# Performance work log

Hardware: AMD Instinct MI355X
Metric: run time of the kernel (lower is better)

The kernel has to match this reference:

```python
import jax, jax.numpy as jnp
import numpy as np

N = 40000          # nodes
E = 640000         # edges (avg degree 16)
D_MODEL = 128
H = 8              # num_heads
DH = 16            # d_head
DFF = 512
CLAMP = 5.0
EPS = 1e-5


def setup_inputs() -> dict:
    key = jax.random.key(0)
    ks = jax.random.split(key, 10)
    s = 0.08  # weight init scale
    return {
        "feat": jax.random.normal(ks[0], (N, D_MODEL), dtype=jnp.float32),
        "src": jax.random.randint(ks[1], (E,), 0, N, dtype=jnp.int32),
        "dst": jax.random.randint(ks[2], (E,), 0, N, dtype=jnp.int32),
        "Wq": jax.random.normal(ks[3], (H * DH, D_MODEL), dtype=jnp.float32) * s,
        "Wk": jax.random.normal(ks[4], (H * DH, D_MODEL), dtype=jnp.float32) * s,
        "Wv": jax.random.normal(ks[5], (H * DH, D_MODEL), dtype=jnp.float32) * s,
        "Wo": jax.random.normal(ks[6], (D_MODEL, H * DH), dtype=jnp.float32) * s,
        "ln1_g": jnp.ones((D_MODEL,), jnp.float32),
        "ln1_b": jnp.zeros((D_MODEL,), jnp.float32),
        "W1": jax.random.normal(ks[7], (DFF, D_MODEL), dtype=jnp.float32) * s,
        "b1": jnp.zeros((DFF,), jnp.float32),
        "W2": jax.random.normal(ks[8], (D_MODEL, DFF), dtype=jnp.float32) * s,
        "b2": jnp.zeros((D_MODEL,), jnp.float32),
        "ln2_g": jnp.ones((D_MODEL,), jnp.float32),
        "ln2_b": jnp.zeros((D_MODEL,), jnp.float32),
    }


def _layer_norm(x, g, b):
    mu = jnp.mean(x, axis=-1, keepdims=True)
    var = jnp.mean(jnp.square(x - mu), axis=-1, keepdims=True)
    return (x - mu) * jax.lax.rsqrt(var + EPS) * g + b


def reference(feat, src, dst, Wq, Wk, Wv, Wo, ln1_g, ln1_b, W1, b1, W2, b2, ln2_g, ln2_b):
    n = feat.shape[0]
    # Node-level projections (equivalent to DGL's per-edge Linear on gathered feats)
    q = (feat @ Wq.T).reshape(n, H, DH)
    k = (feat @ Wk.T).reshape(n, H, DH)
    v = (feat @ Wv.T).reshape(n, H, DH)

    # Per-edge multi-head attention logits: q[dst] . k[src] / sqrt(d_head), clamped
    u = jnp.sum(q[dst] * k[src], axis=-1) / np.sqrt(DH)   # [E, H]
    u = jnp.clip(u, -CLAMP, CLAMP)

    # Ragged edge-softmax over incoming edges of each dst node
    m = jax.ops.segment_max(u, dst, num_segments=n)        # [N, H]
    e = jnp.exp(u - m[dst])                                # [E, H]
    denom = jax.ops.segment_sum(e, dst, num_segments=n)    # [N, H]
    a = e / denom[dst]                                     # [E, H]

    # Weighted V scatter-reduce back to dst nodes
    av = (a[:, :, None] * v[src]).reshape(-1, H * DH)      # [E, H*DH]
    sum_av = jax.ops.segment_sum(av, dst, num_segments=n)  # [N, H*DH]
    uh = sum_av @ Wo.T                                     # [N, d_model]

    h1 = _layer_norm(feat + uh, ln1_g, ln1_b)
    ffn = jax.nn.relu(h1 @ W1.T + b1) @ W2.T + b2
    return _layer_norm(h1 + ffn, ln2_g, ln2_b)
```

## Files before the change

kernel.cpp:

```cpp
#include <hip/hip_runtime.h>

#define DM 128
#define DFF 512
#define CLAMP_V 5.0f
#define LN_EPS 1e-5f

typedef __attribute__((ext_vector_type(8))) short bf16x8;
typedef __attribute__((ext_vector_type(4))) float f32x4;

__device__ __forceinline__ float b2f(ushort u) {
  union { uint u; float f; } x; x.u = ((uint)u) << 16; return x.f;
}
__device__ __forceinline__ ushort f2b(float f) {
  union { float f; uint u; } x; x.f = f;
  uint r = x.u + 0x7FFFu + ((x.u >> 16) & 1u);
  return (ushort)(r >> 16);
}
__device__ __forceinline__ void unpackw(uint w, float& lo, float& hi) {
  union { uint u; float f; } A, B;
  A.u = w << 16; B.u = w & 0xFFFF0000u;
  lo = A.f; hi = B.f;
}
__device__ __forceinline__ void unpack8w(uint4 w, float* o) {
  unpackw(w.x, o[0], o[1]); unpackw(w.y, o[2], o[3]);
  unpackw(w.z, o[4], o[5]); unpackw(w.w, o[6], o[7]);
}

__global__ void k_prep(const float* __restrict__ feat,
                       const float* __restrict__ wq, const float* __restrict__ wk,
                       const float* __restrict__ wv, const float* __restrict__ wo,
                       const float* __restrict__ w1, const float* __restrict__ w2,
                       ushort* __restrict__ feat_bf, ushort* __restrict__ wbf,
                       const int* __restrict__ dst, int* __restrict__ deg,
                       int nf4, int castBlocks, int E) {
  if ((int)blockIdx.x >= castBlocks) {
    int e = ((int)blockIdx.x - castBlocks) * 256 + threadIdx.x;
    if (e < E) atomicAdd(&deg[dst[e]], 1);
    return;
  }
  int i = blockIdx.x * 256 + threadIdx.x;
  if (i < nf4) {
    float4 v = *reinterpret_cast<const float4*>(feat + i * 4);
    ushort4 o; o.x = f2b(v.x); o.y = f2b(v.y); o.z = f2b(v.z); o.w = f2b(v.w);
    *reinterpret_cast<ushort4*>(feat_bf + i * 4) = o;
    return;
  }
  int i4 = (i - nf4) * 4;
  if (i4 >= 196608) return;
  const float* s; int o;
  if      (i4 < 16384)  { s = wq; o = i4; }
  else if (i4 < 32768)  { s = wk; o = i4 - 16384; }
  else if (i4 < 49152)  { s = wv; o = i4 - 32768; }
  else if (i4 < 65536)  { s = wo; o = i4 - 49152; }
  else if (i4 < 131072) { s = w1; o = i4 - 65536; }
  else                  { s = w2; o = i4 - 131072; }
  float4 v = *reinterpret_cast<const float4*>(s + o);
  ushort4 u; u.x = f2b(v.x); u.y = f2b(v.y); u.z = f2b(v.z); u.w = f2b(v.w);
  *reinterpret_cast<ushort4*>(wbf + i4) = u;
}

#define SC_EPB 1024

__global__ __launch_bounds__(256) void k_scan(const int* __restrict__ deg,
                                              int* __restrict__ off,
                                              int* __restrict__ cur,
                                              int n, int E) {
  __shared__ int sh[256];
  __shared__ int wsum[4];
  const int t = threadIdx.x;
  const int bstart = blockIdx.x * SC_EPB;

  int gs = 0;
  for (int base = t * 4; base < bstart; base += SC_EPB) {
    int4 v = *reinterpret_cast<const int4*>(deg + base);
    gs += v.x + v.y + v.z + v.w;
  }
  #pragma unroll
  for (int m = 1; m < 64; m <<= 1) gs += __shfl_xor(gs, m);
  if ((t & 63) == 0) wsum[t >> 6] = gs;
  __syncthreads();
  int gadd = wsum[0] + wsum[1] + wsum[2] + wsum[3];
  __syncthreads();

  int base = bstart + t * 4;
  int4 v = {0, 0, 0, 0};
  if (base + 3 < n) {
    v = *reinterpret_cast<const int4*>(deg + base);
  } else {
    if (base     < n) v.x = deg[base];
    if (base + 1 < n) v.y = deg[base + 1];
    if (base + 2 < n) v.z = deg[base + 2];
    if (base + 3 < n) v.w = deg[base + 3];
  }
  int s = v.x + v.y + v.z + v.w;
  sh[t] = s;
  __syncthreads();
  #pragma unroll
  for (int d = 1; d < 256; d <<= 1) {
    int x = 0;
    if (t >= d) x = sh[t - d];
    __syncthreads();
    sh[t] += x;
    __syncthreads();
  }
  int ex = sh[t] - s + gadd;
  if (base + 3 < n) {
    int4 o; o.x = ex; o.y = ex + v.x; o.z = ex + v.x + v.y; o.w = ex + v.x + v.y + v.z;
    *reinterpret_cast<int4*>(off + base) = o;
    int4 z = {0, 0, 0, 0};
    *reinterpret_cast<int4*>(cur + base) = z;
  } else {
    if (base     < n) { off[base]     = ex;                    cur[base]     = 0; }
    if (base + 1 < n) { off[base + 1] = ex + v.x;              cur[base + 1] = 0; }
    if (base + 2 < n) { off[base + 2] = ex + v.x + v.y;        cur[base + 2] = 0; }
    if (base + 3 < n) { off[base + 3] = ex + v.x + v.y + v.z;  cur[base + 3] = 0; }
  }
  if (blockIdx.x == 0 && t == 0) off[n] = E;
}

__global__ void k_scatter(const int* __restrict__ src, const int* __restrict__ dst,
                          const int* __restrict__ off, int* __restrict__ cur,
                          int* __restrict__ csr, int E) {
  int e = blockIdx.x * blockDim.x + threadIdx.x;
  if (e < E) {
    int d = dst[e];
    int p = off[d] + atomicAdd(&cur[d], 1);
    csr[p] = src[e];
  }
}

template<int FLAGS>
__global__ __launch_bounds__(512, 2) void k_mmT(
    const ushort* __restrict__ A, const ushort* __restrict__ W,
    ushort* __restrict__ Cb, ushort* __restrict__ Cb2, int M)
{
  __shared__ ushort As[128 * 128];
  __shared__ ushort Bs[128 * 128];

  const int tid = threadIdx.x;
  const int wv = tid >> 6, ln = tid & 63;
  const int bnb = blockIdx.x;
  const int mbase = blockIdx.y * 128;
  const int wrow = (wv >> 2) * 64, wcol = (wv & 3) * 32;
  const int o_base = tid * 16;

  #pragma unroll
  for (int is = 0; is < 4; ++is) {
    int o = is * 8192 + o_base;
    int row = o >> 8;
    int c = ((o >> 4) & 15) ^ (row & 15);
    int gr = min(mbase + row, M - 1);
    const ushort* sA = A + (size_t)gr * 128 + c * 8;
    __builtin_amdgcn_global_load_lds(
        (const __attribute__((address_space(1))) void*)sA,
        (__attribute__((address_space(3))) void*)((char*)As + is * 8192 + wv * 1024),
        16, 0, 0);
    const ushort* sB = W + (size_t)(bnb * 128 + row) * 128 + c * 8;
    __builtin_amdgcn_global_load_lds(
        (const __attribute__((address_space(1))) void*)sB,
        (__attribute__((address_space(3))) void*)((char*)Bs + is * 8192 + wv * 1024),
        16, 0, 0);
  }
  __syncthreads();

  f32x4 acc[4][2] = {};
  const char* AsB = (const char*)As;
  const char* BsB = (const char*)Bs;
  #pragma unroll
  for (int kk = 0; kk < 4; ++kk) {
    bf16x8 af[4], bfr[2];
    #pragma unroll
    for (int m = 0; m < 4; ++m) {
      int r = wrow + m * 16 + (ln & 15);
      int c = kk * 4 + (ln >> 4);
      af[m] = *reinterpret_cast<const bf16x8*>(AsB + r * 256 + ((c ^ (r & 15)) << 4));
    }
    #pragma unroll
    for (int n = 0; n < 2; ++n) {
      int r = wcol + n * 16 + (ln & 15);
      int c = kk * 4 + (ln >> 4);
      bfr[n] = *reinterpret_cast<const bf16x8*>(BsB + r * 256 + ((c ^ (r & 15)) << 4));
    }
    #pragma unroll
    for (int m = 0; m < 4; ++m)
      #pragma unroll
      for (int n = 0; n < 2; ++n)
        acc[m][n] = __builtin_amdgcn_mfma_f32_16x16x32_bf16(af[m], bfr[n], acc[m][n], 0, 0, 0);
  }

  #pragma unroll
  for (int m = 0; m < 4; ++m) {
    int gr0 = mbase + wrow + m * 16 + (ln >> 4) * 4;
    #pragma unroll
    for (int n = 0; n < 2; ++n) {
      int gcl = wcol + n * 16 + (ln & 15);
      #pragma unroll
      for (int r = 0; r < 4; ++r) {
        int gr = gr0 + r;
        if (gr >= M) continue;
        float v = acc[m][n][r];
        if (bnb == 0) Cb[(size_t)gr * 128 + gcl] = f2b(v);
        else          Cb2[(size_t)gr * 256 + (bnb - 1) * 128 + gcl] = f2b(v);
      }
    }
  }
}

__global__ __launch_bounds__(512, 2) void k_fused(
    const ushort* __restrict__ sav, const float* __restrict__ feat,
    const ushort* __restrict__ wo,
    const float* __restrict__ ln1g, const float* __restrict__ ln1b,
    const ushort* __restrict__ w1, const float* __restrict__ b1,
    const ushort* __restrict__ w2, const float* __restrict__ b2,
    const float* __restrict__ ln2g, const float* __restrict__ ln2b,
    float* __restrict__ outp, int M)
{
  __shared__ ushort mid[64 * 512];
  __shared__ ushort wbuf[2][128 * 128];

  const int tid = threadIdx.x;
  const int wv = tid >> 6, ln = tid & 63;
  const int lr = ln & 15, hi = ln >> 4;
  const int mbase = blockIdx.x * 64;
  char* M0 = (char*)mid;
  char* M1 = (char*)mid + 16384;
  char* M2 = (char*)mid + 32768;

  auto STG128 = [&](const ushort* srcBase, int srcLd, int colOff, char* dstLds) {
    #pragma unroll
    for (int is = 0; is < 4; ++is) {
      int o = is * 8192 + tid * 16;
      int r = o >> 8;
      int c = ((o >> 4) & 15) ^ (r & 15);
      const ushort* s = srcBase + (size_t)r * srcLd + colOff + c * 8;
      __builtin_amdgcn_global_load_lds(
          (const __attribute__((address_space(1))) void*)s,
          (__attribute__((address_space(3))) void*)(dstLds + is * 8192 + wv * 1024),
          16, 0, 0);
    }
  };

  #pragma unroll
  for (int is = 0; is < 2; ++is) {
    int o = is * 8192 + tid * 16;
    int r = o >> 8;
    int c = ((o >> 4) & 15) ^ (r & 15);
    int gr = min(mbase + r, M - 1);
    const ushort* s = sav + (size_t)gr * 128 + c * 8;
    __builtin_amdgcn_global_load_lds(
        (const __attribute__((address_space(1))) void*)s,
        (__attribute__((address_space(3))) void*)(M1 + is * 8192 + wv * 1024),
        16, 0, 0);
  }
  STG128(wo, 128, 0, (char*)wbuf[0]);
  STG128(w1, 128, 0, M2);
  __syncthreads();

  const int gc = wv * 16 + lr;

  f32x4 p0[4] = {};
  {
    const char* wB = (const char*)wbuf[0];
    #pragma unroll
    for (int kk = 0; kk < 4; ++kk) {
      int c = kk * 4 + hi;
      int wr = wv * 16 + lr;
      bf16x8 bWo = *reinterpret_cast<const bf16x8*>(wB + wr * 256 + ((c ^ (wr & 15)) << 4));
      bf16x8 aS[4];
      #pragma unroll
      for (int m = 0; m < 4; ++m) {
        int r = m * 16 + lr;
        aS[m] = *reinterpret_cast<const bf16x8*>(M1 + r * 256 + ((c ^ (r & 15)) << 4));
      }
      #pragma unroll
      for (int m = 0; m < 4; ++m)
        p0[m] = __builtin_amdgcn_mfma_f32_16x16x32_bf16(aS[m], bWo, p0[m], 0, 0, 0);
    }
  }
  #pragma unroll
  for (int m = 0; m < 4; ++m)
    #pragma unroll
    for (int r = 0; r < 4; ++r) {
      int gr = mbase + m * 16 + hi * 4 + r;
      p0[m][r] += feat[(size_t)min(gr, M - 1) * 128 + gc];
    }
  float* lnred = reinterpret_cast<float*>(&wbuf[1][0]);
  #pragma unroll
  for (int m = 0; m < 4; ++m)
    #pragma unroll
    for (int r = 0; r < 4; ++r) {
      float sm = p0[m][r];
      float sq = p0[m][r] * p0[m][r];
      #pragma unroll
      for (int msk = 1; msk <= 8; msk <<= 1) {
        sm += __shfl_xor(sm, msk);
        sq += __shfl_xor(sq, msk);
      }
      if (lr == 0) {
        int row = m * 16 + hi * 4 + r;
        lnred[row * 16 + wv * 2]     = sm;
        lnred[row * 16 + wv * 2 + 1] = sq;
      }
    }
  __syncthreads();
  STG128(w1 + 16384, 128, 0, (char*)wbuf[0]);
  {
    float g1v = ln1g[gc], bb1 = ln1b[gc];
    int chunk = gc >> 3;
    int sub = (gc & 7) * 2;
    #pragma unroll
    for (int m = 0; m < 4; ++m)
      #pragma unroll
      for (int r = 0; r < 4; ++r) {
        int row = m * 16 + hi * 4 + r;
        float sm = 0.f, sq = 0.f;
        #pragma unroll
        for (int w = 0; w < 8; ++w) {
          sm += lnred[row * 16 + w * 2];
          sq += lnred[row * 16 + w * 2 + 1];
        }
        float mu = sm * (1.f / 128.f);
        float var = fmaxf(sq * (1.f / 128.f) - mu * mu, 0.f);
        float rstd = rsqrtf(var + LN_EPS);
        float y = (p0[m][r] - mu) * rstd * g1v + bb1;
        p0[m][r] = y;
        *reinterpret_cast<ushort*>(M0 + row * 256 + ((chunk ^ (row & 15)) << 4) + sub) = f2b(y);
      }
  }
  __syncthreads();

  f32x4 p1[4][4] = {};
  #pragma unroll
  for (int g = 0; g < 4; ++g) {
    if (g == 0) STG128(w1 + 2 * 16384, 128, 0, (char*)wbuf[1]);
    if (g == 1) STG128(w1 + 3 * 16384, 128, 0, M2);
    if (g == 2) STG128(w2, 512, 0,   (char*)wbuf[0]);
    if (g == 3) STG128(w2, 512, 128, (char*)wbuf[1]);
    const char* wB = (g == 0) ? M2
                   : (g == 1) ? (const char*)wbuf[0]
                   : (g == 2) ? (const char*)wbuf[1]
                   : M2;
    #pragma unroll
    for (int kk = 0; kk < 4; ++kk) {
      int c = kk * 4 + hi;
      int wr = wv * 16 + lr;
      bf16x8 aW = *reinterpret_cast<const bf16x8*>(wB + wr * 256 + ((c ^ (wr & 15)) << 4));
      bf16x8 bH[4];
      #pragma unroll
      for (int hj = 0; hj < 4; ++hj) {
        int r = hj * 16 + lr;
        bH[hj] = *reinterpret_cast<const bf16x8*>(M0 + r * 256 + ((c ^ (r & 15)) << 4));
      }
      #pragma unroll
      for (int hj = 0; hj < 4; ++hj)
        p1[g][hj] = __builtin_amdgcn_mfma_f32_16x16x32_bf16(aW, bH[hj], p1[g][hj], 0, 0, 0);
    }
    __syncthreads();
  }

  #pragma unroll
  for (int g = 0; g < 4; ++g) {
    int mc0 = g * 128 + wv * 16 + hi * 4;
    float4 bv = *reinterpret_cast<const float4*>(b1 + mc0);
    int chunk = mc0 >> 3;
    int sub = (mc0 & 7) * 2;
    #pragma unroll
    for (int hj = 0; hj < 4; ++hj) {
      int orow = hj * 16 + lr;
      ushort4 pk;
      pk.x = f2b(fmaxf(p1[g][hj][0] + bv.x, 0.f));
      pk.y = f2b(fmaxf(p1[g][hj][1] + bv.y, 0.f));
      pk.z = f2b(fmaxf(p1[g][hj][2] + bv.z, 0.f));
      pk.w = f2b(fmaxf(p1[g][hj][3] + bv.w, 0.f));
      char* dstp = (char*)mid + orow * 1024 + (((chunk & 63) ^ (orow & 15)) << 4) + sub;
      *reinterpret_cast<ushort4*>(dstp) = pk;
    }
  }
  __syncthreads();

  f32x4 p2[4] = {};
  #pragma unroll
  for (int g2 = 0; g2 < 4; ++g2) {
    if (g2 == 1) STG128(w2, 512, 256, (char*)wbuf[0]);
    if (g2 == 2) STG128(w2, 512, 384, (char*)wbuf[1]);
    const char* wB = (const char*)wbuf[g2 & 1];
    #pragma unroll
    for (int kk = 0; kk < 4; ++kk) {
      int wr = wv * 16 + lr;
      int cw = kk * 4 + hi;
      bf16x8 bW = *reinterpret_cast<const bf16x8*>(wB + wr * 256 + ((cw ^ (wr & 15)) << 4));
      int cm = g2 * 16 + kk * 4 + hi;
      bf16x8 aM[4];
      #pragma unroll
      for (int m = 0; m < 4; ++m) {
        int r = m * 16 + lr;
        aM[m] = *reinterpret_cast<const bf16x8*>((const char*)mid + r * 1024 + (((cm & 63) ^ (r & 15)) << 4));
      }
      #pragma unroll
      for (int m = 0; m < 4; ++m)
        p2[m] = __builtin_amdgcn_mfma_f32_16x16x32_bf16(aM[m], bW, p2[m], 0, 0, 0);
    }
    __syncthreads();
  }

  lnred = reinterpret_cast<float*>(&wbuf[0][0]);
  {
    float bsv = b2[gc];
    #pragma unroll
    for (int m = 0; m < 4; ++m)
      #pragma unroll
      for (int r = 0; r < 4; ++r)
        p2[m][r] += bsv + p0[m][r];
  }
  #pragma unroll
  for (int m = 0; m < 4; ++m)
    #pragma unroll
    for (int r = 0; r < 4; ++r) {
      float sm = p2[m][r];
      float sq = p2[m][r] * p2[m][r];
      #pragma unroll
      for (int msk = 1; msk <= 8; msk <<= 1) {
        sm += __shfl_xor(sm, msk);
        sq += __shfl_xor(sq, msk);
      }
      if (lr == 0) {
        int row = m * 16 + hi * 4 + r;
        lnred[row * 16 + wv * 2]     = sm;
        lnred[row * 16 + wv * 2 + 1] = sq;
      }
    }
  __syncthreads();
  {
    float g2v = ln2g[gc], bb2 = ln2b[gc];
    #pragma unroll
    for (int m = 0; m < 4; ++m)
      #pragma unroll
      for (int r = 0; r < 4; ++r) {
        int row = m * 16 + hi * 4 + r;
        int gr = mbase + row;
        float sm = 0.f, sq = 0.f;
        #pragma unroll
        for (int w = 0; w < 8; ++w) {
          sm += lnred[row * 16 + w * 2];
          sq += lnred[row * 16 + w * 2 + 1];
        }
        float mu = sm * (1.f / 128.f);
        float var = fmaxf(sq * (1.f / 128.f) - mu * mu, 0.f);
        float rstd = rsqrtf(var + LN_EPS);
        if (gr < M)
          outp[(size_t)gr * 128 + gc] = (p2[m][r] - mu) * rstd * g2v + bb2;
      }
  }
}

__global__ __launch_bounds__(256) void k_attn(
    const ushort* __restrict__ q, const ushort* __restrict__ kv,
    const int* __restrict__ off, const int* __restrict__ csr,
    ushort* __restrict__ sav, int n)
{
  int node = blockIdx.x * 4 + (threadIdx.x >> 6);
  int lane = threadIdx.x & 63;
  if (node >= n) return;
  const int g = lane >> 3, sl = lane & 7;

  const ushort* qr = q + (size_t)node * 128 + sl * 16;
  uint4 qw0 = *reinterpret_cast<const uint4*>(qr);
  uint4 qw1 = *reinterpret_cast<const uint4*>(qr + 8);
  float qv[16];
  unpack8w(qw0, qv); unpack8w(qw1, qv + 8);

  int b = off[node], e = off[node + 1];
  float s = 0.f;
  float a[16] = {};
  int nIt = (e - b + 7) >> 3;
  int idx = b + g;
  int sn = (b < e) ? csr[min(idx, e - 1)] : 0;

  for (int i = 0; i < nIt; ++i) {
    bool act = idx < e;
    const ushort* kr = kv + (size_t)sn * 256 + sl * 16;
    uint4 kw0 = *reinterpret_cast<const uint4*>(kr);
    uint4 kw1 = *reinterpret_cast<const uint4*>(kr + 8);
    uint4 vw0 = *reinterpret_cast<const uint4*>(kr + 128);
    uint4 vw1 = *reinterpret_cast<const uint4*>(kr + 136);
    idx += 8;
    if (i + 1 < nIt) sn = csr[min(idx, e - 1)];

    float kk[16];
    unpack8w(kw0, kk); unpack8w(kw1, kk + 8);
    float p = 0.f;
    #pragma unroll
    for (int j = 0; j < 16; ++j) p = fmaf(qv[j], kk[j], p);
    float u = fminf(fmaxf(p * 0.25f, -CLAMP_V), CLAMP_V);
    float w = __expf(u - CLAMP_V);
    w = act ? w : 0.f;
    s += w;
    float vvv[16];
    unpack8w(vw0, vvv); unpack8w(vw1, vvv + 8);
    #pragma unroll
    for (int j = 0; j < 16; ++j) a[j] = fmaf(w, vvv[j], a[j]);
  }

  #pragma unroll
  for (int msk = 8; msk <= 32; msk <<= 1) {
    s += __shfl_xor(s, msk);
    #pragma unroll
    for (int j = 0; j < 16; ++j) a[j] += __shfl_xor(a[j], msk);
  }

  float inv = (s > 0.f) ? 1.f / s : 0.f;
  if (g == 0) {
    uint w[8];
    #pragma unroll
    for (int j = 0; j < 8; ++j)
      w[j] = (uint)f2b(a[2 * j] * inv) | ((uint)f2b(a[2 * j + 1] * inv) << 16);
    ushort* outp = sav + (size_t)node * 128 + sl * 16;
    uint4 o0 = {w[0], w[1], w[2], w[3]};
    uint4 o1 = {w[4], w[5], w[6], w[7]};
    *reinterpret_cast<uint4*>(outp) = o0;
    *reinterpret_cast<uint4*>(outp + 8) = o1;
  }
}

extern "C" void kernel_launch(void* const* d_in, const int* in_sizes, int n_in,
                              void* d_out, int out_size, void* d_ws, size_t ws_size,
                              hipStream_t stream)
{
  const float* feat = (const float*)d_in[0];
  const int*   src  = (const int*)d_in[1];
  const int*   dst  = (const int*)d_in[2];
  const float* Wq   = (const float*)d_in[3];
  const float* Wk   = (const float*)d_in[4];
  const float* Wv   = (const float*)d_in[5];
  const float* Wo   = (const float*)d_in[6];
  const float* ln1g = (const float*)d_in[7];
  const float* ln1b = (const float*)d_in[8];
  const float* W1   = (const float*)d_in[9];
  const float* b1   = (const float*)d_in[10];
  const float* W2   = (const float*)d_in[11];
  const float* b2   = (const float*)d_in[12];
  const float* ln2g = (const float*)d_in[13];
  const float* ln2b = (const float*)d_in[14];
  float* out = (float*)d_out;

  const int N = in_sizes[0] / DM;
  const int E = in_sizes[1];
  const size_t NB = (size_t)N;

  char* wsb = (char*)d_ws;
  ushort* q_bf    = (ushort*)wsb;
  ushort* kv_bf   = (ushort*)(wsb + NB * 256);
  ushort* sav_bf  = (ushort*)(wsb + NB * 768);
  ushort* feat_bf = (ushort*)(wsb + NB * 1792);
  ushort* wbf     = (ushort*)(wsb + NB * 2048);
  ushort* wqkv_bf = wbf;
  ushort* wo_bf   = wbf + 49152;
  ushort* w1_bf   = wbf + 65536;
  ushort* w2_bf   = wbf + 131072;
  int* ib  = (int*)(wbf + 196608);
  int* deg = ib;
  int* cur = ib + N;
  int* off = ib + 2 * N;
  int* csr = ib + 3 * N + 1;

  hipMemsetAsync(deg, 0, (size_t)N * sizeof(int), stream);

  int nf4 = N * DM / 4;
  int castBlocks = (nf4 + 49152 + 255) / 256;
  int cntBlocks = (E + 255) / 256;
  k_prep<<<castBlocks + cntBlocks, 256, 0, stream>>>(
      feat, Wq, Wk, Wv, Wo, W1, W2, feat_bf, wbf, dst, deg, nf4, castBlocks, E);

  int nbk = (N + SC_EPB - 1) / SC_EPB;
  k_scan<<<nbk, 256, 0, stream>>>(deg, off, cur, N, E);
  k_scatter<<<cntBlocks, 256, 0, stream>>>(src, dst, off, cur, csr, E);

  int nb4 = (N + 3) / 4;
  const int nT = (N + 127) / 128;

  k_mmT<0><<<dim3(3, nT), 512, 0, stream>>>(feat_bf, wqkv_bf, q_bf, kv_bf, N);

  k_attn<<<nb4, 256, 0, stream>>>(q_bf, kv_bf, off, csr, sav_bf, N);

  const int nF = (N + 63) / 64;
  k_fused<<<nF, 512, 0, stream>>>(
      sav_bf, feat, wo_bf, ln1g, ln1b, w1_bf, b1, w2_bf, b2, ln2g, ln2b, out, N);
}
```

Baseline: 196.8 us.

## Merge CSR scatter into QKV GEMM, split out-proj+LN1 kernel, packed-f32 attention

The CSR scatter pass now runs as extra blocks of the QKV projection launch, which removes one kernel launch and lets the two overlap. The Wo projection, residual add and LayerNorm1 move out of the fused FFN kernel into a separate GEMM+LN kernel with 128-row tiles, which writes h1 in bf16. The FFN kernel then reads h1 back and uses a simpler double-buffered weight staging. The attention inner loop is rewritten with float2 vectors so the compiler can emit packed FP32 FMAs. The split adds a global round-trip of h1 and an extra launch, and using the bf16 h1 as the residual slightly changes numerics.

```diff
diff --git a/kernel.cpp b/kernel.cpp
--- a/kernel.cpp
+++ b/kernel.cpp
@@ -7,6 +7,7 @@
 
 typedef __attribute__((ext_vector_type(8))) short bf16x8;
 typedef __attribute__((ext_vector_type(4))) float f32x4;
+typedef __attribute__((ext_vector_type(2))) float f32x2;
 
 __device__ __forceinline__ float b2f(ushort u) {
   union { uint u; float f; } x; x.u = ((uint)u) << 16; return x.f;
@@ -16,14 +17,10 @@
   uint r = x.u + 0x7FFFu + ((x.u >> 16) & 1u);
   return (ushort)(r >> 16);
 }
-__device__ __forceinline__ void unpackw(uint w, float& lo, float& hi) {
-  union { uint u; float f; } A, B;
-  A.u = w << 16; B.u = w & 0xFFFF0000u;
-  lo = A.f; hi = B.f;
-}
-__device__ __forceinline__ void unpack8w(uint4 w, float* o) {
-  unpackw(w.x, o[0], o[1]); unpackw(w.y, o[2], o[3]);
-  unpackw(w.z, o[4], o[5]); unpackw(w.w, o[6], o[7]);
+__device__ __forceinline__ f32x2 upk2(uint w) {
+  union { uint u; float f; } a, b;
+  a.u = w << 16; b.u = w & 0xFFFF0000u;
+  f32x2 r; r[0] = a.f; r[1] = b.f; return r;
 }
 
 __global__ void k_prep(const float* __restrict__ feat,
@@ -118,29 +115,30 @@
   if (blockIdx.x == 0 && t == 0) off[n] = E;
 }
 
-__global__ void k_scatter(const int* __restrict__ src, const int* __restrict__ dst,
-                          const int* __restrict__ off, int* __restrict__ cur,
-                          int* __restrict__ csr, int E) {
-  int e = blockIdx.x * blockDim.x + threadIdx.x;
-  if (e < E) {
-    int d = dst[e];
-    int p = off[d] + atomicAdd(&cur[d], 1);
-    csr[p] = src[e];
-  }
-}
-
-template<int FLAGS>
-__global__ __launch_bounds__(512, 2) void k_mmT(
+__global__ __launch_bounds__(512, 2) void k_sqkv(
     const ushort* __restrict__ A, const ushort* __restrict__ W,
-    ushort* __restrict__ Cb, ushort* __restrict__ Cb2, int M)
+    ushort* __restrict__ Cb, ushort* __restrict__ Cb2, int M,
+    const int* __restrict__ src, const int* __restrict__ dst,
+    const int* __restrict__ off, int* __restrict__ cur,
+    int* __restrict__ csr, int E, int qkvB)
 {
   __shared__ ushort As[128 * 128];
   __shared__ ushort Bs[128 * 128];
 
+  if ((int)blockIdx.x >= qkvB) {
+    int e = ((int)blockIdx.x - qkvB) * 512 + threadIdx.x;
+    if (e < E) {
+      int d = dst[e];
+      int p = off[d] + atomicAdd(&cur[d], 1);
+      csr[p] = src[e];
+    }
+    return;
+  }
+
   const int tid = threadIdx.x;
   const int wv = tid >> 6, ln = tid & 63;
-  const int bnb = blockIdx.x;
-  const int mbase = blockIdx.y * 128;
+  const int bnb = blockIdx.x % 3;
+  const int mbase = (blockIdx.x / 3) * 128;
   const int wrow = (wv >> 2) * 64, wcol = (wv & 3) * 32;
   const int o_base = tid * 16;
 
@@ -206,13 +204,126 @@
   }
 }
 
-__global__ __launch_bounds__(512, 2) void k_fused(
-    const ushort* __restrict__ sav, const float* __restrict__ feat,
-    const ushort* __restrict__ wo,
-    const float* __restrict__ ln1g, const float* __restrict__ ln1b,
+template<int FLAGS, bool OUTF, bool OUTB>
+__global__ __launch_bounds__(512, 2) void k_mmT(
+    const ushort* __restrict__ A, const ushort* __restrict__ W,
+    const float* __restrict__ res,
+    const float* __restrict__ lng, const float* __restrict__ lnbv,
+    float* __restrict__ Cf, ushort* __restrict__ Cb, int M)
+{
+  __shared__ ushort As[128 * 128];
+  __shared__ ushort Bs[128 * 128];
+  __shared__ float lnred[1024];
+
+  const int tid = threadIdx.x;
+  const int wv = tid >> 6, ln = tid & 63;
+  const int mbase = blockIdx.y * 128;
+  const int wrow = (wv >> 2) * 64, wcol = (wv & 3) * 32;
+  const int o_base = tid * 16;
+
+  #pragma unroll
+  for (int is = 0; is < 4; ++is) {
+    int o = is * 8192 + o_base;
+    int row = o >> 8;
+    int c = ((o >> 4) & 15) ^ (row & 15);
+    int gr = min(mbase + row, M - 1);
+    const ushort* sA = A + (size_t)gr * 128 + c * 8;
+    __builtin_amdgcn_global_load_lds(
+        (const __attribute__((address_space(1))) void*)sA,
+        (__attribute__((address_space(3))) void*)((char*)As + is * 8192 + wv * 1024),
+        16, 0, 0);
+    const ushort* sB = W + (size_t)row * 128 + c * 8;
+    __builtin_amdgcn_global_load_lds(
+        (const __attribute__((address_space(1))) void*)sB,
+        (__attribute__((address_space(3))) void*)((char*)Bs + is * 8192 + wv * 1024),
+        16, 0, 0);
+  }
+  __syncthreads();
+
+  f32x4 acc[4][2] = {};
+  const char* AsB = (const char*)As;
+  const char* BsB = (const char*)Bs;
+  #pragma unroll
+  for (int kk = 0; kk < 4; ++kk) {
+    bf16x8 af[4], bfr[2];
+    #pragma unroll
+    for (int m = 0; m < 4; ++m) {
+      int r = wrow + m * 16 + (ln & 15);
+      int c = kk * 4 + (ln >> 4);
+      af[m] = *reinterpret_cast<const bf16x8*>(AsB + r * 256 + ((c ^ (r & 15)) << 4));
+    }
+    #pragma unroll
+    for (int n = 0; n < 2; ++n) {
+      int r = wcol + n * 16 + (ln & 15);
+      int c = kk * 4 + (ln >> 4);
+      bfr[n] = *reinterpret_cast<const bf16x8*>(BsB + r * 256 + ((c ^ (r & 15)) << 4));
+    }
+    #pragma unroll
+    for (int m = 0; m < 4; ++m)
+      #pragma unroll
+      for (int n = 0; n < 2; ++n)
+        acc[m][n] = __builtin_amdgcn_mfma_f32_16x16x32_bf16(af[m], bfr[n], acc[m][n], 0, 0, 0);
+  }
+
+  #pragma unroll
+  for (int m = 0; m < 4; ++m)
+    #pragma unroll
+    for (int n = 0; n < 2; ++n) {
+      int gc = wcol + n * 16 + (ln & 15);
+      #pragma unroll
+      for (int r = 0; r < 4; ++r) {
+        int gr = mbase + wrow + m * 16 + (ln >> 4) * 4 + r;
+        float v = acc[m][n][r];
+        if (FLAGS & 4) v += res[(size_t)min(gr, M - 1) * 128 + gc];
+        acc[m][n][r] = v;
+      }
+    }
+  #pragma unroll
+  for (int m = 0; m < 4; ++m)
+    #pragma unroll
+    for (int r = 0; r < 4; ++r) {
+      float sm = acc[m][0][r] + acc[m][1][r];
+      float sq = acc[m][0][r] * acc[m][0][r] + acc[m][1][r] * acc[m][1][r];
+      #pragma unroll
+      for (int msk = 1; msk <= 8; msk <<= 1) {
+        sm += __shfl_xor(sm, msk);
+        sq += __shfl_xor(sq, msk);
+      }
+      if ((ln & 15) == 0) {
+        int row = wrow + m * 16 + (ln >> 4) * 4 + r;
+        lnred[row * 8 + (wv & 3) * 2]     = sm;
+        lnred[row * 8 + (wv & 3) * 2 + 1] = sq;
+      }
+    }
+  __syncthreads();
+  #pragma unroll
+  for (int m = 0; m < 4; ++m)
+    #pragma unroll
+    for (int r = 0; r < 4; ++r) {
+      int row = wrow + m * 16 + (ln >> 4) * 4 + r;
+      int gr = mbase + row;
+      float sm = lnred[row * 8] + lnred[row * 8 + 2] + lnred[row * 8 + 4] + lnred[row * 8 + 6];
+      float sq = lnred[row * 8 + 1] + lnred[row * 8 + 3] + lnred[row * 8 + 5] + lnred[row * 8 + 7];
+      float mu = sm * (1.f / 128.f);
+      float var = fmaxf(sq * (1.f / 128.f) - mu * mu, 0.f);
+      float rstd = rsqrtf(var + LN_EPS);
+      if (gr < M) {
+        #pragma unroll
+        for (int n = 0; n < 2; ++n) {
+          int gc = wcol + n * 16 + (ln & 15);
+          float y = (acc[m][n][r] - mu) * rstd * lng[gc] + lnbv[gc];
+          if (OUTF) Cf[(size_t)gr * 128 + gc] = y;
+          if (OUTB) Cb[(size_t)gr * 128 + gc] = f2b(y);
+        }
+      }
+    }
+}
+
+__global__ __launch_bounds__(512, 2) void k_ffn(
+    const ushort* __restrict__ h1b,
     const ushort* __restrict__ w1, const float* __restrict__ b1,
     const ushort* __restrict__ w2, const float* __restrict__ b2,
-    const float* __restrict__ ln2g, const float* __restrict__ ln2b,
+    const float* __restrict__ lng, const float* __restrict__ lnbv,
     float* __restrict__ outp, int M)
 {
   __shared__ ushort mid[64 * 512];
@@ -222,9 +333,7 @@
   const int wv = tid >> 6, ln = tid & 63;
   const int lr = ln & 15, hi = ln >> 4;
   const int mbase = blockIdx.x * 64;
-  char* M0 = (char*)mid;
-  char* M1 = (char*)mid + 16384;
-  char* M2 = (char*)mid + 32768;
+  const int gc = wv * 16 + lr;
 
   auto STG128 = [&](const ushort* srcBase, int srcLd, int colOff, char* dstLds) {
     #pragma unroll
@@ -246,100 +355,23 @@
     int r = o >> 8;
     int c = ((o >> 4) & 15) ^ (r & 15);
     int gr = min(mbase + r, M - 1);
-    const ushort* s = sav + (size_t)gr * 128 + c * 8;
+    const ushort* s = h1b + (size_t)gr * 128 + c * 8;
     __builtin_amdgcn_global_load_lds(
         (const __attribute__((address_space(1))) void*)s,
-        (__attribute__((address_space(3))) void*)(M1 + is * 8192 + wv * 1024),
+        (__attribute__((address_space(3))) void*)((char*)mid + is * 8192 + wv * 1024),
         16, 0, 0);
   }
-  STG128(wo, 128, 0, (char*)wbuf[0]);
-  STG128(w1, 128, 0, M2);
-  __syncthreads();
-
-  const int gc = wv * 16 + lr;
-
-  f32x4 p0[4] = {};
-  {
-    const char* wB = (const char*)wbuf[0];
-    #pragma unroll
-    for (int kk = 0; kk < 4; ++kk) {
-      int c = kk * 4 + hi;
-      int wr = wv * 16 + lr;
-      bf16x8 bWo = *reinterpret_cast<const bf16x8*>(wB + wr * 256 + ((c ^ (wr & 15)) << 4));
-      bf16x8 aS[4];
-      #pragma unroll
-      for (int m = 0; m < 4; ++m) {
-        int r = m * 16 + lr;
-        aS[m] = *reinterpret_cast<const bf16x8*>(M1 + r * 256 + ((c ^ (r & 15)) << 4));
-      }
-      #pragma unroll
-      for (int m = 0; m < 4; ++m)
-        p0[m] = __builtin_amdgcn_mfma_f32_16x16x32_bf16(aS[m], bWo, p0[m], 0, 0, 0);
-    }
-  }
-  #pragma unroll
-  for (int m = 0; m < 4; ++m)
-    #pragma unroll
-    for (int r = 0; r < 4; ++r) {
-      int gr = mbase + m * 16 + hi * 4 + r;
-      p0[m][r] += feat[(size_t)min(gr, M - 1) * 128 + gc];
-    }
-  float* lnred = reinterpret_cast<float*>(&wbuf[1][0]);
-  #pragma unroll
-  for (int m = 0; m < 4; ++m)
-    #pragma unroll
-    for (int r = 0; r < 4; ++r) {
-      float sm = p0[m][r];
-      float sq = p0[m][r] * p0[m][r];
-      #pragma unroll
-      for (int msk = 1; msk <= 8; msk <<= 1) {
-        sm += __shfl_xor(sm, msk);
-        sq += __shfl_xor(sq, msk);
-      }
-      if (lr == 0) {
-        int row = m * 16 + hi * 4 + r;
-        lnred[row * 16 + wv * 2]     = sm;
-        lnred[row * 16 + wv * 2 + 1] = sq;
-      }
-    }
-  __syncthreads();
-  STG128(w1 + 16384, 128, 0, (char*)wbuf[0]);
-  {
-    float g1v = ln1g[gc], bb1 = ln1b[gc];
-    int chunk = gc >> 3;
-    int sub = (gc & 7) * 2;
-    #pragma unroll
-    for (int m = 0; m < 4; ++m)
-      #pragma unroll
-      for (int r = 0; r < 4; ++r) {
-        int row = m * 16 + hi * 4 + r;
-        float sm = 0.f, sq = 0.f;
-        #pragma unroll
-        for (int w = 0; w < 8; ++w) {
-          sm += lnred[row * 16 + w * 2];
-          sq += lnred[row * 16 + w * 2 + 1];
-        }
-        float mu = sm * (1.f / 128.f);
-        float var = fmaxf(sq * (1.f / 128.f) - mu * mu, 0.f);
-        float rstd = rsqrtf(var + LN_EPS);
-        float y = (p0[m][r] - mu) * rstd * g1v + bb1;
-        p0[m][r] = y;
-        *reinterpret_cast<ushort*>(M0 + row * 256 + ((chunk ^ (row & 15)) << 4) + sub) = f2b(y);
-      }
-  }
+  STG128(w1, 128, 0, (char*)wbuf[0]);
   __syncthreads();
 
   f32x4 p1[4][4] = {};
+  const char* hB = (const char*)mid;
   #pragma unroll
   for (int g = 0; g < 4; ++g) {
-    if (g == 0) STG128(w1 + 2 * 16384, 128, 0, (char*)wbuf[1]);
-    if (g == 1) STG128(w1 + 3 * 16384, 128, 0, M2);
-    if (g == 2) STG128(w2, 512, 0,   (char*)wbuf[0]);
-    if (g == 3) STG128(w2, 512, 128, (char*)wbuf[1]);
-    const char* wB = (g == 0) ? M2
-                   : (g == 1) ? (const char*)wbuf[0]
-                   : (g == 2) ? (const char*)wbuf[1]
-                   : M2;
+    const int buf = g & 1;
+    if (g < 3) STG128(w1 + (size_t)(g + 1) * 128 * 128, 128, 0, (char*)wbuf[buf ^ 1]);
+    else       STG128(w2, 512, 0, (char*)wbuf[buf ^ 1]);
+    const char* wB = (const char*)wbuf[buf];
     #pragma unroll
     for (int kk = 0; kk < 4; ++kk) {
       int c = kk * 4 + hi;
@@ -349,7 +381,7 @@
       #pragma unroll
       for (int hj = 0; hj < 4; ++hj) {
         int r = hj * 16 + lr;
-        bH[hj] = *reinterpret_cast<const bf16x8*>(M0 + r * 256 + ((c ^ (r & 15)) << 4));
+        bH[hj] = *reinterpret_cast<const bf16x8*>(hB + r * 256 + ((c ^ (r & 15)) << 4));
       }
       #pragma unroll
       for (int hj = 0; hj < 4; ++hj)
@@ -357,6 +389,21 @@
     }
     __syncthreads();
   }
+
+  float h1res[4][4];
+  {
+    int chunk = gc >> 3;
+    int sub = (gc & 7) * 2;
+    #pragma unroll
+    for (int m = 0; m < 4; ++m)
+      #pragma unroll
+      for (int r = 0; r < 4; ++r) {
+        int row = m * 16 + hi * 4 + r;
+        h1res[m][r] = b2f(*reinterpret_cast<const ushort*>(
+            (const char*)mid + row * 256 + ((chunk ^ (row & 15)) << 4) + sub));
+      }
+  }
+  __syncthreads();
 
   #pragma unroll
   for (int g = 0; g < 4; ++g) {
@@ -381,9 +428,9 @@
   f32x4 p2[4] = {};
   #pragma unroll
   for (int g2 = 0; g2 < 4; ++g2) {
-    if (g2 == 1) STG128(w2, 512, 256, (char*)wbuf[0]);
-    if (g2 == 2) STG128(w2, 512, 384, (char*)wbuf[1]);
-    const char* wB = (const char*)wbuf[g2 & 1];
+    const int buf = g2 & 1;
+    if (g2 < 3) STG128(w2, 512, (g2 + 1) * 128, (char*)wbuf[buf ^ 1]);
+    const char* wB = (const char*)wbuf[buf];
     #pragma unroll
     for (int kk = 0; kk < 4; ++kk) {
       int wr = wv * 16 + lr;
@@ -403,14 +450,14 @@
     __syncthreads();
   }
 
-  lnred = reinterpret_cast<float*>(&wbuf[0][0]);
+  float* lnred = reinterpret_cast<float*>(&wbuf[0][0]);
   {
     float bsv = b2[gc];
     #pragma unroll
     for (int m = 0; m < 4; ++m)
       #pragma unroll
       for (int r = 0; r < 4; ++r)
-        p2[m][r] += bsv + p0[m][r];
+        p2[m][r] += bsv + h1res[m][r];
   }
   #pragma unroll
   for (int m = 0; m < 4; ++m)
@@ -431,7 +478,7 @@
     }
   __syncthreads();
   {
-    float g2v = ln2g[gc], bb2 = ln2b[gc];
+    float g2v = lng[gc], bb2 = lnbv[gc];
     #pragma unroll
     for (int m = 0; m < 4; ++m)
       #pragma unroll
@@ -466,12 +513,13 @@
   const ushort* qr = q + (size_t)node * 128 + sl * 16;
   uint4 qw0 = *reinterpret_cast<const uint4*>(qr);
   uint4 qw1 = *reinterpret_cast<const uint4*>(qr + 8);
-  float qv[16];
-  unpack8w(qw0, qv); unpack8w(qw1, qv + 8);
+  f32x2 qv[8];
+  qv[0] = upk2(qw0.x); qv[1] = upk2(qw0.y); qv[2] = upk2(qw0.z); qv[3] = upk2(qw0.w);
+  qv[4] = upk2(qw1.x); qv[5] = upk2(qw1.y); qv[6] = upk2(qw1.z); qv[7] = upk2(qw1.w);
 
   int b = off[node], e = off[node + 1];
   float s = 0.f;
-  float a[16] = {};
+  f32x2 a2[8] = {};
   int nIt = (e - b + 7) >> 3;
   int idx = b + g;
   int sn = (b < e) ? csr[min(idx, e - 1)] : 0;
@@ -486,26 +534,38 @@
     idx += 8;
     if (i + 1 < nIt) sn = csr[min(idx, e - 1)];
 
-    float kk[16];
-    unpack8w(kw0, kk); unpack8w(kw1, kk + 8);
-    float p = 0.f;
-    #pragma unroll
-    for (int j = 0; j < 16; ++j) p = fmaf(qv[j], kk[j], p);
+    f32x2 acc = qv[0] * upk2(kw0.x);
+    acc += qv[1] * upk2(kw0.y);
+    acc += qv[2] * upk2(kw0.z);
+    acc += qv[3] * upk2(kw0.w);
+    acc += qv[4] * upk2(kw1.x);
+    acc += qv[5] * upk2(kw1.y);
+    acc += qv[6] * upk2(kw1.z);
+    acc += qv[7] * upk2(kw1.w);
+    float p = acc[0] + acc[1];
     float u = fminf(fmaxf(p * 0.25f, -CLAMP_V), CLAMP_V);
     float w = __expf(u - CLAMP_V);
     w = act ? w : 0.f;
     s += w;
-    float vvv[16];
-    unpack8w(vw0, vvv); unpack8w(vw1, vvv + 8);
-    #pragma unroll
-    for (int j = 0; j < 16; ++j) a[j] = fmaf(w, vvv[j], a[j]);
+    f32x2 w2; w2[0] = w; w2[1] = w;
+    a2[0] += w2 * upk2(vw0.x);
+    a2[1] += w2 * upk2(vw0.y);
+    a2[2] += w2 * upk2(vw0.z);
+    a2[3] += w2 * upk2(vw0.w);
+    a2[4] += w2 * upk2(vw1.x);
+    a2[5] += w2 * upk2(vw1.y);
+    a2[6] += w2 * upk2(vw1.z);
+    a2[7] += w2 * upk2(vw1.w);
   }
 
   #pragma unroll
   for (int msk = 8; msk <= 32; msk <<= 1) {
     s += __shfl_xor(s, msk);
     #pragma unroll
-    for (int j = 0; j < 16; ++j) a[j] += __shfl_xor(a[j], msk);
+    for (int j = 0; j < 8; ++j) {
+      a2[j][0] += __shfl_xor(a2[j][0], msk);
+      a2[j][1] += __shfl_xor(a2[j][1], msk);
+    }
   }
 
   float inv = (s > 0.f) ? 1.f / s : 0.f;
@@ -513,7 +573,7 @@
     uint w[8];
     #pragma unroll
     for (int j = 0; j < 8; ++j)
-      w[j] = (uint)f2b(a[2 * j] * inv) | ((uint)f2b(a[2 * j + 1] * inv) << 16);
+      w[j] = (uint)f2b(a2[j][0] * inv) | ((uint)f2b(a2[j][1] * inv) << 16);
     ushort* outp = sav + (size_t)node * 128 + sl * 16;
     uint4 o0 = {w[0], w[1], w[2], w[3]};
     uint4 o1 = {w[4], w[5], w[6], w[7]};
@@ -551,6 +611,7 @@
   ushort* q_bf    = (ushort*)wsb;
   ushort* kv_bf   = (ushort*)(wsb + NB * 256);
   ushort* sav_bf  = (ushort*)(wsb + NB * 768);
+  ushort* h1b     = (ushort*)(wsb + NB * 1536);
   ushort* feat_bf = (ushort*)(wsb + NB * 1792);
   ushort* wbf     = (ushort*)(wsb + NB * 2048);
   ushort* wqkv_bf = wbf;
@@ -573,16 +634,20 @@
 
   int nbk = (N + SC_EPB - 1) / SC_EPB;
   k_scan<<<nbk, 256, 0, stream>>>(deg, off, cur, N, E);
-  k_scatter<<<cntBlocks, 256, 0, stream>>>(src, dst, off, cur, csr, E);
+
+  const int nT = (N + 127) / 128;
+  int qkvB = 3 * nT;
+  int scB = (E + 511) / 512;
+  k_sqkv<<<qkvB + scB, 512, 0, stream>>>(
+      feat_bf, wqkv_bf, q_bf, kv_bf, N, src, dst, off, cur, csr, E, qkvB);
 
   int nb4 = (N + 3) / 4;
-  const int nT = (N + 127) / 128;
-
-  k_mmT<0><<<dim3(3, nT), 512, 0, stream>>>(feat_bf, wqkv_bf, q_bf, kv_bf, N);
-
   k_attn<<<nb4, 256, 0, stream>>>(q_bf, kv_bf, off, csr, sav_bf, N);
 
+  k_mmT<4 | 8, false, true><<<dim3(1, nT), 512, 0, stream>>>(
+      sav_bf, wo_bf, feat, ln1g, ln1b, nullptr, h1b, N);
+
   const int nF = (N + 63) / 64;
-  k_fused<<<nF, 512, 0, stream>>>(
-      sav_bf, feat, wo_bf, ln1g, ln1b, w1_bf, b1, w2_bf, b2, ln2g, ln2b, out, N);
-}
+  k_ffn<<<nF, 512, 0, stream>>>(
+      h1b, w1_bf, b1, w2_bf, b2, ln2g, ln2b, out, N);
+}
```

Result: faster. 192.2 us (-2.3%).
